# Performance work log

Hardware: AMD Instinct MI355X
Metric: run time of the kernel (lower is better)

The kernel has to match this reference:

```python
import jax, jax.numpy as jnp
import numpy as np

NUM_EXPERTS = 8
TOP_K = 2


def setup_inputs() -> dict:
    key = jax.random.key(0)
    k0, k1, k2, k3, k4 = jax.random.split(key, 5)
    T, D, F, E = 4096, 2048, 4096, NUM_EXPERTS  # tokens, hidden, intermediate, experts
    s_in = 1.0 / np.sqrt(D).astype(np.float32)
    s_mid = 1.0 / np.sqrt(F).astype(np.float32)
    return {
        "hidden_states": jax.random.normal(k0, (T, D), jnp.float32),
        "gate_w": jax.random.normal(k1, (D, E), jnp.float32) * s_in,   # router gate (no bias)
        "w1": jax.random.normal(k2, (E, D, F), jnp.float32) * s_in,     # expert gate proj
        "w3": jax.random.normal(k3, (E, D, F), jnp.float32) * s_in,     # expert up proj
        "w2": jax.random.normal(k4, (E, F, D), jnp.float32) * s_mid,    # expert down proj
    }


def reference(hidden_states, gate_w, w1, w3, w2):
    x = hidden_states  # [T, D] (original flattens any leading dims)
    # Router: logits in fp32 (router_logits.float()), softmax over ALL experts,
    # take top-k WITHOUT renormalization (renormalize=False).
    logits = (x @ gate_w).astype(jnp.float32)            # [T, E]
    probs = jax.nn.softmax(logits, axis=-1)              # [T, E]
    topk_w, topk_i = jax.lax.top_k(probs, TOP_K)         # [T, K]
    # Dense combine weights: zero for non-selected experts. [T, E]
    combine = jnp.sum(
        jax.nn.one_hot(topk_i, NUM_EXPERTS, dtype=x.dtype) * topk_w[..., None],
        axis=1,
    )

    # SwiGLU experts, vmapped over the expert axis (fixed, small E).
    def expert_fn(w1e, w3e, w2e):
        return (jax.nn.silu(x @ w1e) * (x @ w3e)) @ w2e  # [T, D]

    expert_out = jax.vmap(expert_fn)(w1, w3, w2)         # [E, T, D]
    return jnp.einsum("te,etd->td", combine, expert_out)  # [T, D]
```

## Files before the change

### kernel.cpp

```cpp
#include <hip/hip_runtime.h>
#include <hip/hip_bf16.h>

#define TK 4096
#define DD 2048
#define FF 4096
#define NE 8
#define BM 128
#define BN 128
#define BK 32

typedef __attribute__((ext_vector_type(8))) short bf16x8;
typedef __attribute__((ext_vector_type(4))) short bf16x4;
typedef __attribute__((ext_vector_type(4))) float f32x4;

__device__ __forceinline__ unsigned short f2bf(float f) {
  return __builtin_bit_cast(unsigned short, __float2bfloat16(f));
}

__device__ __forceinline__ int g_swz(int row) { return ((row >> 1) & 3) ^ ((row >> 3) & 3); }
__device__ __forceinline__ int swzoff(int row, int bir) {
  return row * 64 + ((((bir >> 4) ^ g_swz(row)) & 3) << 4) + (bir & 15);
}
__device__ __forceinline__ int permB(int f) {
  return (f & 0x60) | ((f & 3) << 3) | ((f >> 2) & 7);
}

__global__ void k_router(const float* __restrict__ x, const float* __restrict__ gw,
                         int* __restrict__ cnt, int* __restrict__ ltok,
                         float* __restrict__ lw) {
  int tok = (blockIdx.x * blockDim.x + threadIdx.x) >> 6;
  int lane = threadIdx.x & 63;
  if (tok >= TK) return;
  const float* xr = x + (size_t)tok * DD;
  float a0=0,a1=0,a2=0,a3=0,a4=0,a5=0,a6=0,a7=0;
  for (int p = 0; p < DD / 256; ++p) {
    int d0 = p * 256 + lane * 4;
    f32x4 xv = *(const f32x4*)(xr + d0);
#pragma unroll
    for (int j = 0; j < 4; ++j) {
      float xs = xv[j];
      const f32x4* g = (const f32x4*)(gw + (size_t)(d0 + j) * NE);
      f32x4 g0 = g[0], g1 = g[1];
      a0 += xs * g0[0]; a1 += xs * g0[1]; a2 += xs * g0[2]; a3 += xs * g0[3];
      a4 += xs * g1[0]; a5 += xs * g1[1]; a6 += xs * g1[2]; a7 += xs * g1[3];
    }
  }
#pragma unroll
  for (int s = 32; s > 0; s >>= 1) {
    a0 += __shfl_xor(a0, s, 64); a1 += __shfl_xor(a1, s, 64);
    a2 += __shfl_xor(a2, s, 64); a3 += __shfl_xor(a3, s, 64);
    a4 += __shfl_xor(a4, s, 64); a5 += __shfl_xor(a5, s, 64);
    a6 += __shfl_xor(a6, s, 64); a7 += __shfl_xor(a7, s, 64);
  }
  if (lane == 0) {
    float p_[NE] = {a0, a1, a2, a3, a4, a5, a6, a7};
    float m = p_[0];
#pragma unroll
    for (int e = 1; e < NE; ++e) m = fmaxf(m, p_[e]);
    float ssum = 0.f;
#pragma unroll
    for (int e = 0; e < NE; ++e) { p_[e] = __expf(p_[e] - m); ssum += p_[e]; }
    float inv = 1.f / ssum;
    int i1 = 0; float b1 = p_[0];
#pragma unroll
    for (int e = 1; e < NE; ++e) if (p_[e] > b1) { b1 = p_[e]; i1 = e; }
    int i2 = -1; float b2 = -1.f;
#pragma unroll
    for (int e = 0; e < NE; ++e) if (e != i1 && p_[e] > b2) { b2 = p_[e]; i2 = e; }
    int s1 = atomicAdd(&cnt[i1], 1);
    ltok[i1 * TK + s1] = tok; lw[i1 * TK + s1] = b1 * inv;
    int s2 = atomicAdd(&cnt[i2], 1);
    ltok[i2 * TK + s2] = tok; lw[i2 * TK + s2] = b2 * inv;
  }
}

__global__ void k_prefix(const int* __restrict__ cnt, int* __restrict__ off) {
  if (threadIdx.x == 0) {
    int a = 0;
#pragma unroll
    for (int e = 0; e < NE; ++e) { off[e] = a; a += cnt[e]; }
    off[NE] = a;
  }
}

__global__ __launch_bounds__(256, 2)
void k_gemm1(const float* __restrict__ x, const float* __restrict__ w1g,
             const float* __restrict__ w3g, const int* __restrict__ cnt,
             const int* __restrict__ off, const int* __restrict__ ltok,
             const float* __restrict__ lw, unsigned short* __restrict__ H) {
  const int e = blockIdx.z;
  const int ce = cnt[e];
  const int m0 = blockIdx.y * BM;
  if (m0 >= ce) return;
  const int n0 = blockIdx.x * BN;
  const int tid = threadIdx.x, lane = tid & 63, wv = tid >> 6;
  const int wr = wv >> 1, wc = wv & 1;
  const float* W1 = w1g + (size_t)e * DD * FF;
  const float* W3 = w3g + (size_t)e * DD * FF;
  const int base = off[e];

  __shared__ unsigned short As[2][BM * BK];
  __shared__ unsigned short B1s[2][BN * BK];
  __shared__ unsigned short B3s[2][BN * BK];

  const int arow = tid >> 1, ah = tid & 1;
  const float* xrow = (m0 + arow < ce) ? (x + (size_t)ltok[e * TK + (m0 + arow)] * DD) : nullptr;
  const int dblk = tid >> 5, fblk = tid & 31;

  const int kb = (lane >> 4) * 16;
  int aOff[4], bOff[4], wAoff[4], wBoff[4];
#pragma unroll
  for (int m = 0; m < 4; ++m) aOff[m] = swzoff(wr * 64 + m * 16 + (lane & 15), kb);
#pragma unroll
  for (int n = 0; n < 4; ++n) bOff[n] = swzoff(permB(wc * 64 + n * 16 + (lane & 15)), kb);
#pragma unroll
  for (int j = 0; j < 4; ++j) {
    wAoff[j] = swzoff(arow, ah * 32 + j * 8);
    wBoff[j] = swzoff(permB(fblk * 4 + j), dblk * 8);
  }

  f32x4 acc1[4][4], acc3[4][4];
#pragma unroll
  for (int m = 0; m < 4; ++m)
#pragma unroll
    for (int n = 0; n < 4; ++n)
#pragma unroll
      for (int j = 0; j < 4; ++j) { acc1[m][n][j] = 0.f; acc3[m][n][j] = 0.f; }

  f32x4 av[4], v1[4], v3[4];

  auto LOAD = [&](int kt) {
    const int k0 = kt * BK;
#pragma unroll
    for (int j = 0; j < 4; ++j) {
      if (xrow) av[j] = *(const f32x4*)(xrow + k0 + ah * 16 + j * 4);
      else { av[j][0] = 0.f; av[j][1] = 0.f; av[j][2] = 0.f; av[j][3] = 0.f; }
    }
    const float* p1 = W1 + (size_t)(k0 + dblk * 4) * FF + (n0 + fblk * 4);
    const float* p3 = W3 + (size_t)(k0 + dblk * 4) * FF + (n0 + fblk * 4);
#pragma unroll
    for (int r = 0; r < 4; ++r) {
      v1[r] = *(const f32x4*)(p1 + (size_t)r * FF);
      v3[r] = *(const f32x4*)(p3 + (size_t)r * FF);
    }
  };
  auto STORE = [&](int buf) {
#pragma unroll
    for (int j = 0; j < 4; ++j) {
      bf16x4 t;
      t[0] = (short)f2bf(av[j][0]); t[1] = (short)f2bf(av[j][1]);
      t[2] = (short)f2bf(av[j][2]); t[3] = (short)f2bf(av[j][3]);
      *(bf16x4*)((char*)As[buf] + wAoff[j]) = t;
    }
#pragma unroll
    for (int j = 0; j < 4; ++j) {
      bf16x4 t1, t3;
      t1[0] = (short)f2bf(v1[0][j]); t1[1] = (short)f2bf(v1[1][j]);
      t1[2] = (short)f2bf(v1[2][j]); t1[3] = (short)f2bf(v1[3][j]);
      t3[0] = (short)f2bf(v3[0][j]); t3[1] = (short)f2bf(v3[1][j]);
      t3[2] = (short)f2bf(v3[2][j]); t3[3] = (short)f2bf(v3[3][j]);
      *(bf16x4*)((char*)B1s[buf] + wBoff[j]) = t1;
      *(bf16x4*)((char*)B3s[buf] + wBoff[j]) = t3;
    }
  };

  LOAD(0);
  STORE(0);
  int cur = 0;
  const int NT = DD / BK;
  for (int kt = 0; kt < NT; ++kt) {
    if (kt + 1 < NT) LOAD(kt + 1);
    __syncthreads();
    bf16x8 af[4];
#pragma unroll
    for (int m = 0; m < 4; ++m) af[m] = *(const bf16x8*)((const char*)As[cur] + aOff[m]);
#pragma unroll
    for (int n = 0; n < 4; ++n) {
      bf16x8 b1 = *(const bf16x8*)((const char*)B1s[cur] + bOff[n]);
      bf16x8 b3 = *(const bf16x8*)((const char*)B3s[cur] + bOff[n]);
#pragma unroll
      for (int m = 0; m < 4; ++m) {
        acc1[m][n] = __builtin_amdgcn_mfma_f32_16x16x32_bf16(af[m], b1, acc1[m][n], 0, 0, 0);
        acc3[m][n] = __builtin_amdgcn_mfma_f32_16x16x32_bf16(af[m], b3, acc3[m][n], 0, 0, 0);
      }
    }
    if (kt + 1 < NT) STORE(cur ^ 1);
    cur ^= 1;
  }

#pragma unroll
  for (int m = 0; m < 4; ++m) {
    const int rbase = wr * 64 + m * 16 + ((lane >> 4) << 2);
    float wts[4]; bool val[4];
#pragma unroll
    for (int j = 0; j < 4; ++j) {
      int r = m0 + rbase + j;
      val[j] = r < ce;
      wts[j] = val[j] ? lw[e * TK + r] : 0.f;
    }
#pragma unroll
    for (int n = 0; n < 4; ++n) {
      const int col = n0 + wc * 64 + n * 16 + (lane & 15);
#pragma unroll
      for (int j = 0; j < 4; ++j) {
        if (!val[j]) continue;
        float s1 = acc1[m][n][j], s3 = acc3[m][n][j];
        float h = s1 / (1.f + __expf(-s1)) * s3 * wts[j];
        H[(size_t)(base + m0 + rbase + j) * FF + col] = f2bf(h);
      }
    }
  }
}

__global__ __launch_bounds__(256, 2)
void k_gemm2(const unsigned short* __restrict__ H, const float* __restrict__ w2g,
             const int* __restrict__ cnt, const int* __restrict__ off,
             const int* __restrict__ ltok, float* __restrict__ out) {
  const int e = blockIdx.z;
  const int ce = cnt[e];
  const int m0 = blockIdx.y * BM;
  if (m0 >= ce) return;
  const int n0 = blockIdx.x * BN;
  const int tid = threadIdx.x, lane = tid & 63, wv = tid >> 6;
  const int wr = wv >> 1, wc = wv & 1;
  const float* W2 = w2g + (size_t)e * FF * DD;
  const int base = off[e];

  __shared__ unsigned short As[2][BM * BK];
  __shared__ unsigned short Bs[2][BN * BK];

  const int arow = tid >> 1, ah = tid & 1;
  const bool aval = (m0 + arow) < ce;
  const unsigned short* hrow = H + (size_t)(base + m0 + arow) * FF;
  const int kblk = tid >> 5, nblk = tid & 31;

  const int kb = (lane >> 4) * 16;
  int aOff[4], bOff[4], wAoff[2], wBoff[4];
#pragma unroll
  for (int m = 0; m < 4; ++m) aOff[m] = swzoff(wr * 64 + m * 16 + (lane & 15), kb);
#pragma unroll
  for (int n = 0; n < 4; ++n) bOff[n] = swzoff(permB(wc * 64 + n * 16 + (lane & 15)), kb);
#pragma unroll
  for (int j = 0; j < 2; ++j) wAoff[j] = swzoff(arow, ah * 32 + j * 16);
#pragma unroll
  for (int j = 0; j < 4; ++j) wBoff[j] = swzoff(permB(nblk * 4 + j), kblk * 8);

  f32x4 acc[4][4];
#pragma unroll
  for (int m = 0; m < 4; ++m)
#pragma unroll
    for (int n = 0; n < 4; ++n)
#pragma unroll
      for (int j = 0; j < 4; ++j) acc[m][n][j] = 0.f;

  bf16x8 av2[2];
  f32x4 wv2[4];

  auto LOAD = [&](int kt) {
    const int k0 = kt * BK;
#pragma unroll
    for (int j = 0; j < 2; ++j) {
      if (aval) av2[j] = *(const bf16x8*)(hrow + k0 + ah * 16 + j * 8);
      else {
#pragma unroll
        for (int q = 0; q < 8; ++q) av2[j][q] = 0;
      }
    }
    const float* p = W2 + (size_t)(k0 + kblk * 4) * DD + (n0 + nblk * 4);
#pragma unroll
    for (int r = 0; r < 4; ++r) wv2[r] = *(const f32x4*)(p + (size_t)r * DD);
  };
  auto STORE = [&](int buf) {
#pragma unroll
    for (int j = 0; j < 2; ++j) *(bf16x8*)((char*)As[buf] + wAoff[j]) = av2[j];
#pragma unroll
    for (int j = 0; j < 4; ++j) {
      bf16x4 t;
      t[0] = (short)f2bf(wv2[0][j]); t[1] = (short)f2bf(wv2[1][j]);
      t[2] = (short)f2bf(wv2[2][j]); t[3] = (short)f2bf(wv2[3][j]);
      *(bf16x4*)((char*)Bs[buf] + wBoff[j]) = t;
    }
  };

  LOAD(0);
  STORE(0);
  int cur = 0;
  const int NT = FF / BK;
  for (int kt = 0; kt < NT; ++kt) {
    if (kt + 1 < NT) LOAD(kt + 1);
    __syncthreads();
    bf16x8 af[4];
#pragma unroll
    for (int m = 0; m < 4; ++m) af[m] = *(const bf16x8*)((const char*)As[cur] + aOff[m]);
#pragma unroll
    for (int n = 0; n < 4; ++n) {
      bf16x8 bf = *(const bf16x8*)((const char*)Bs[cur] + bOff[n]);
#pragma unroll
      for (int m = 0; m < 4; ++m)
        acc[m][n] = __builtin_amdgcn_mfma_f32_16x16x32_bf16(af[m], bf, acc[m][n], 0, 0, 0);
    }
    if (kt + 1 < NT) STORE(cur ^ 1);
    cur ^= 1;
  }

#pragma unroll
  for (int m = 0; m < 4; ++m) {
    const int rbase = wr * 64 + m * 16 + ((lane >> 4) << 2);
    int toks[4]; bool val[4];
#pragma unroll
    for (int j = 0; j < 4; ++j) {
      int r = m0 + rbase + j;
      val[j] = r < ce;
      toks[j] = val[j] ? ltok[e * TK + r] : 0;
    }
#pragma unroll
    for (int n = 0; n < 4; ++n) {
      const int col = n0 + wc * 64 + n * 16 + (lane & 15);
#pragma unroll
      for (int j = 0; j < 4; ++j)
        if (val[j]) atomicAdd(out + (size_t)toks[j] * DD + col, acc[m][n][j]);
    }
  }
}

extern "C" void kernel_launch(void* const* d_in, const int* in_sizes, int n_in,
                              void* d_out, int out_size, void* d_ws, size_t ws_size,
                              hipStream_t stream) {
  const float* x  = (const float*)d_in[0];
  const float* gw = (const float*)d_in[1];
  const float* w1 = (const float*)d_in[2];
  const float* w3 = (const float*)d_in[3];
  const float* w2 = (const float*)d_in[4];
  float* out = (float*)d_out;

  char* ws = (char*)d_ws;
  int*   cnt  = (int*)(ws);
  int*   off  = (int*)(ws + 64);
  int*   ltok = (int*)(ws + 256);
  float* lw   = (float*)(ws + 256 + (size_t)NE * TK * 4);
  unsigned short* H = (unsigned short*)(ws + (1 << 20));
  const size_t need = (1u << 20) + (size_t)2 * TK * FF * 2;
  if (ws_size < need) return;

  hipMemsetAsync(cnt, 0, 64, stream);
  hipMemsetAsync(d_out, 0, (size_t)out_size * 4, stream);
  k_router<<<dim3(TK / 4), 256, 0, stream>>>(x, gw, cnt, ltok, lw);
  k_prefix<<<dim3(1), 64, 0, stream>>>(cnt, off);
  k_gemm1<<<dim3(FF / BN, TK / BM, NE), 256, 0, stream>>>(x, w1, w3, cnt, off, ltok, lw, H);
  k_gemm2<<<dim3(DD / BN, TK / BM, NE), 256, 0, stream>>>(H, w2, cnt, off, ltok, out);
}
```

Before: 981.7 us.

## Pre-convert weights to transposed bf16 and stream tiles via global_load_lds

```diff
diff --git a/kernel.cpp b/kernel.cpp
--- a/kernel.cpp
+++ b/kernel.cpp
@@ -7,7 +7,8 @@
 #define NE 8
 #define BM 128
 #define BN 128
-#define BK 32
+#define BKR 32
+#define BKG 64
 
 typedef __attribute__((ext_vector_type(8))) short bf16x8;
 typedef __attribute__((ext_vector_type(4))) short bf16x4;
@@ -17,6 +18,12 @@
   return __builtin_bit_cast(unsigned short, __float2bfloat16(f));
 }
 
+__device__ __forceinline__ void gl16(const unsigned short* g, unsigned short* l) {
+  __builtin_amdgcn_global_load_lds(
+      (const __attribute__((address_space(1))) unsigned int*)g,
+      (__attribute__((address_space(3))) unsigned int*)l, 16, 0, 0);
+}
+
 __device__ __forceinline__ int g_swz(int row) { return ((row >> 1) & 3) ^ ((row >> 3) & 3); }
 __device__ __forceinline__ int swzoff(int row, int bir) {
   return row * 64 + ((((bir >> 4) ^ g_swz(row)) & 3) << 4) + (bir & 15);
@@ -27,7 +34,7 @@
 
 __global__ void k_router(const float* __restrict__ x, const float* __restrict__ gw,
                          int* __restrict__ cnt, int* __restrict__ ltok,
-                         float* __restrict__ lw) {
+                         float* __restrict__ lw, unsigned short* __restrict__ xb) {
   int tok = (blockIdx.x * blockDim.x + threadIdx.x) >> 6;
   int lane = threadIdx.x & 63;
   if (tok >= TK) return;
@@ -36,6 +43,12 @@
   for (int p = 0; p < DD / 256; ++p) {
     int d0 = p * 256 + lane * 4;
     f32x4 xv = *(const f32x4*)(xr + d0);
+    if (xb) {
+      bf16x4 t;
+      t[0] = (short)f2bf(xv[0]); t[1] = (short)f2bf(xv[1]);
+      t[2] = (short)f2bf(xv[2]); t[3] = (short)f2bf(xv[3]);
+      *(bf16x4*)(xb + (size_t)tok * DD + d0) = t;
+    }
 #pragma unroll
     for (int j = 0; j < 4; ++j) {
       float xs = xv[j];
@@ -80,6 +93,254 @@
 #pragma unroll
     for (int e = 0; e < NE; ++e) { off[e] = a; a += cnt[e]; }
     off[NE] = a;
+  }
+}
+
+__global__ void k_tr(const float* __restrict__ src0, unsigned short* __restrict__ dst0,
+                     int R, int C) {
+  const int e = blockIdx.z;
+  const float* src = src0 + (size_t)e * R * C;
+  unsigned short* dst = dst0 + (size_t)e * R * C;
+  const int r0 = blockIdx.y * 64, c0 = blockIdx.x * 64;
+  const int tid = threadIdx.x;
+  __shared__ unsigned short t[64][66];
+#pragma unroll
+  for (int p = 0; p < 4; ++p) {
+    int r = p * 16 + (tid >> 4);
+    int c = (tid & 15) * 4;
+    f32x4 v = *(const f32x4*)(src + (size_t)(r0 + r) * C + c0 + c);
+#pragma unroll
+    for (int j = 0; j < 4; ++j) t[c + j][r] = f2bf(v[j]);
+  }
+  __syncthreads();
+#pragma unroll
+  for (int p = 0; p < 2; ++p) {
+    int c = p * 32 + (tid >> 3);
+    int r = (tid & 7) * 8;
+    bf16x8 o;
+#pragma unroll
+    for (int j = 0; j < 8; ++j) o[j] = (short)t[c][r + j];
+    *(bf16x8*)(dst + (size_t)(c0 + c) * R + r0 + r) = o;
+  }
+}
+
+
+__global__ __launch_bounds__(256, 2)
+void k_gemm1g(const unsigned short* __restrict__ xb, const unsigned short* __restrict__ w1t,
+              const unsigned short* __restrict__ w3t, const int* __restrict__ cnt,
+              const int* __restrict__ off, const int* __restrict__ ltok,
+              const float* __restrict__ lw, unsigned short* __restrict__ H) {
+  const int e = blockIdx.z;
+  const int ce = cnt[e];
+  const int m0 = blockIdx.y * BM;
+  if (m0 >= ce) return;
+  const int n0 = blockIdx.x * BN;
+  const int tid = threadIdx.x, lane = tid & 63, w = tid >> 6;
+  const int wr = w >> 1, wc = w & 1;
+  const unsigned short* W1 = w1t + (size_t)e * FF * DD;
+  const unsigned short* W3 = w3t + (size_t)e * FF * DD;
+  const int base = off[e];
+
+  __shared__ __align__(16) unsigned short As[BM * BKG];
+  __shared__ __align__(16) unsigned short B1s[BN * BKG];
+  __shared__ __align__(16) unsigned short B3s[BN * BKG];
+
+  const int swz8 = ((lane & 7) ^ ((lane >> 3) & 7)) * 8;
+  const unsigned short* aSrc[4];
+  const unsigned short* b1Src[4];
+  const unsigned short* b3Src[4];
+#pragma unroll
+  for (int i = 0; i < 4; ++i) {
+    int row = w * 32 + i * 8 + (lane >> 3);
+    int gm = m0 + row;
+    int tok = (gm < ce) ? ltok[e * TK + gm] : 0;
+    aSrc[i]  = xb + (size_t)tok * DD + swz8;
+    b1Src[i] = W1 + (size_t)(n0 + row) * DD + swz8;
+    b3Src[i] = W3 + (size_t)(n0 + row) * DD + swz8;
+  }
+
+  int aOff[4][2], bOff[4][2];
+#pragma unroll
+  for (int m = 0; m < 4; ++m) {
+    int row = wr * 64 + m * 16 + (lane & 15);
+#pragma unroll
+    for (int kk = 0; kk < 2; ++kk) {
+      int c = kk * 4 + (lane >> 4);
+      aOff[m][kk] = row * 128 + ((c ^ (row & 7)) << 4);
+    }
+  }
+#pragma unroll
+  for (int n = 0; n < 4; ++n) {
+    int row = wc * 64 + n * 16 + (lane & 15);
+#pragma unroll
+    for (int kk = 0; kk < 2; ++kk) {
+      int c = kk * 4 + (lane >> 4);
+      bOff[n][kk] = row * 128 + ((c ^ (row & 7)) << 4);
+    }
+  }
+
+  f32x4 acc1[4][4], acc3[4][4];
+#pragma unroll
+  for (int m = 0; m < 4; ++m)
+#pragma unroll
+    for (int n = 0; n < 4; ++n)
+#pragma unroll
+      for (int j = 0; j < 4; ++j) { acc1[m][n][j] = 0.f; acc3[m][n][j] = 0.f; }
+
+  const int NT = DD / BKG;
+  for (int kt = 0; kt < NT; ++kt) {
+#pragma unroll
+    for (int i = 0; i < 4; ++i) {
+      const int seg = w * 4 + i;
+      gl16(aSrc[i],  &As[seg * 512]);
+      gl16(b1Src[i], &B1s[seg * 512]);
+      gl16(b3Src[i], &B3s[seg * 512]);
+      aSrc[i] += BKG; b1Src[i] += BKG; b3Src[i] += BKG;
+    }
+    __syncthreads();
+#pragma unroll
+    for (int kk = 0; kk < 2; ++kk) {
+      bf16x8 af[4];
+#pragma unroll
+      for (int m = 0; m < 4; ++m) af[m] = *(const bf16x8*)((const char*)As + aOff[m][kk]);
+#pragma unroll
+      for (int n = 0; n < 4; ++n) {
+        bf16x8 b1 = *(const bf16x8*)((const char*)B1s + bOff[n][kk]);
+        bf16x8 b3 = *(const bf16x8*)((const char*)B3s + bOff[n][kk]);
+#pragma unroll
+        for (int m = 0; m < 4; ++m) {
+          acc1[m][n] = __builtin_amdgcn_mfma_f32_16x16x32_bf16(af[m], b1, acc1[m][n], 0, 0, 0);
+          acc3[m][n] = __builtin_amdgcn_mfma_f32_16x16x32_bf16(af[m], b3, acc3[m][n], 0, 0, 0);
+        }
+      }
+    }
+    __syncthreads();
+  }
+
+#pragma unroll
+  for (int m = 0; m < 4; ++m) {
+    const int rbase = wr * 64 + m * 16 + ((lane >> 4) << 2);
+    float wts[4]; bool val[4];
+#pragma unroll
+    for (int j = 0; j < 4; ++j) {
+      int r = m0 + rbase + j;
+      val[j] = r < ce;
+      wts[j] = val[j] ? lw[e * TK + r] : 0.f;
+    }
+#pragma unroll
+    for (int n = 0; n < 4; ++n) {
+      const int col = n0 + wc * 64 + n * 16 + (lane & 15);
+#pragma unroll
+      for (int j = 0; j < 4; ++j) {
+        if (!val[j]) continue;
+        float s1 = acc1[m][n][j], s3 = acc3[m][n][j];
+        float h = s1 / (1.f + __expf(-s1)) * s3 * wts[j];
+        H[(size_t)(base + m0 + rbase + j) * FF + col] = f2bf(h);
+      }
+    }
+  }
+}
+
+__global__ __launch_bounds__(256, 3)
+void k_gemm2g(const unsigned short* __restrict__ H, const unsigned short* __restrict__ w2t,
+              const int* __restrict__ cnt, const int* __restrict__ off,
+              const int* __restrict__ ltok, float* __restrict__ out) {
+  const int e = blockIdx.z;
+  const int ce = cnt[e];
+  const int m0 = blockIdx.y * BM;
+  if (m0 >= ce) return;
+  const int n0 = blockIdx.x * BN;
+  const int tid = threadIdx.x, lane = tid & 63, w = tid >> 6;
+  const int wr = w >> 1, wc = w & 1;
+  const unsigned short* W2 = w2t + (size_t)e * DD * FF;
+  const int base = off[e];
+
+  __shared__ __align__(16) unsigned short As[BM * BKG];
+  __shared__ __align__(16) unsigned short Bs[BN * BKG];
+
+  const int swz8 = ((lane & 7) ^ ((lane >> 3) & 7)) * 8;
+  const unsigned short* aSrc[4];
+  const unsigned short* bSrc[4];
+#pragma unroll
+  for (int i = 0; i < 4; ++i) {
+    int row = w * 32 + i * 8 + (lane >> 3);
+    int gm = m0 + row;
+    int hr = (gm < ce) ? gm : 0;
+    aSrc[i] = H + (size_t)(base + hr) * FF + swz8;
+    bSrc[i] = W2 + (size_t)(n0 + row) * FF + swz8;
+  }
+
+  int aOff[4][2], bOff[4][2];
+#pragma unroll
+  for (int m = 0; m < 4; ++m) {
+    int row = wr * 64 + m * 16 + (lane & 15);
+#pragma unroll
+    for (int kk = 0; kk < 2; ++kk) {
+      int c = kk * 4 + (lane >> 4);
+      aOff[m][kk] = row * 128 + ((c ^ (row & 7)) << 4);
+    }
+  }
+#pragma unroll
+  for (int n = 0; n < 4; ++n) {
+    int row = wc * 64 + n * 16 + (lane & 15);
+#pragma unroll
+    for (int kk = 0; kk < 2; ++kk) {
+      int c = kk * 4 + (lane >> 4);
+      bOff[n][kk] = row * 128 + ((c ^ (row & 7)) << 4);
+    }
+  }
+
+  f32x4 acc[4][4];
+#pragma unroll
+  for (int m = 0; m < 4; ++m)
+#pragma unroll
+    for (int n = 0; n < 4; ++n)
+#pragma unroll
+      for (int j = 0; j < 4; ++j) acc[m][n][j] = 0.f;
+
+  const int NT = FF / BKG;
+  for (int kt = 0; kt < NT; ++kt) {
+#pragma unroll
+    for (int i = 0; i < 4; ++i) {
+      const int seg = w * 4 + i;
+      gl16(aSrc[i], &As[seg * 512]);
+      gl16(bSrc[i], &Bs[seg * 512]);
+      aSrc[i] += BKG; bSrc[i] += BKG;
+    }
+    __syncthreads();
+#pragma unroll
+    for (int kk = 0; kk < 2; ++kk) {
+      bf16x8 af[4];
+#pragma unroll
+      for (int m = 0; m < 4; ++m) af[m] = *(const bf16x8*)((const char*)As + aOff[m][kk]);
+#pragma unroll
+      for (int n = 0; n < 4; ++n) {
+        bf16x8 bf = *(const bf16x8*)((const char*)Bs + bOff[n][kk]);
+#pragma unroll
+        for (int m = 0; m < 4; ++m)
+          acc[m][n] = __builtin_amdgcn_mfma_f32_16x16x32_bf16(af[m], bf, acc[m][n], 0, 0, 0);
+      }
+    }
+    __syncthreads();
+  }
+
+#pragma unroll
+  for (int m = 0; m < 4; ++m) {
+    const int rbase = wr * 64 + m * 16 + ((lane >> 4) << 2);
+    int toks[4]; bool val[4];
+#pragma unroll
+    for (int j = 0; j < 4; ++j) {
+      int r = m0 + rbase + j;
+      val[j] = r < ce;
+      toks[j] = val[j] ? ltok[e * TK + r] : 0;
+    }
+#pragma unroll
+    for (int n = 0; n < 4; ++n) {
+      const int col = n0 + wc * 64 + n * 16 + (lane & 15);
+#pragma unroll
+      for (int j = 0; j < 4; ++j)
+        if (val[j]) atomicAdd(out + (size_t)toks[j] * DD + col, acc[m][n][j]);
+    }
   }
 }
 
@@ -99,9 +360,9 @@
   const float* W3 = w3g + (size_t)e * DD * FF;
   const int base = off[e];
 
-  __shared__ unsigned short As[2][BM * BK];
-  __shared__ unsigned short B1s[2][BN * BK];
-  __shared__ unsigned short B3s[2][BN * BK];
+  __shared__ unsigned short As[2][BM * BKR];
+  __shared__ unsigned short B1s[2][BN * BKR];
+  __shared__ unsigned short B3s[2][BN * BKR];
 
   const int arow = tid >> 1, ah = tid & 1;
   const float* xrow = (m0 + arow < ce) ? (x + (size_t)ltok[e * TK + (m0 + arow)] * DD) : nullptr;
@@ -130,7 +391,7 @@
   f32x4 av[4], v1[4], v3[4];
 
   auto LOAD = [&](int kt) {
-    const int k0 = kt * BK;
+    const int k0 = kt * BKR;
 #pragma unroll
     for (int j = 0; j < 4; ++j) {
       if (xrow) av[j] = *(const f32x4*)(xrow + k0 + ah * 16 + j * 4);
@@ -164,10 +425,9 @@
     }
   };
 
-  LOAD(0);
-  STORE(0);
+  LOAD(0); STORE(0);
   int cur = 0;
-  const int NT = DD / BK;
+  const int NT = DD / BKR;
   for (int kt = 0; kt < NT; ++kt) {
     if (kt + 1 < NT) LOAD(kt + 1);
     __syncthreads();
@@ -226,8 +486,8 @@
   const float* W2 = w2g + (size_t)e * FF * DD;
   const int base = off[e];
 
-  __shared__ unsigned short As[2][BM * BK];
-  __shared__ unsigned short Bs[2][BN * BK];
+  __shared__ unsigned short As[2][BM * BKR];
+  __shared__ unsigned short Bs[2][BN * BKR];
 
   const int arow = tid >> 1, ah = tid & 1;
   const bool aval = (m0 + arow) < ce;
@@ -257,7 +517,7 @@
   f32x4 wv2[4];
 
   auto LOAD = [&](int kt) {
-    const int k0 = kt * BK;
+    const int k0 = kt * BKR;
 #pragma unroll
     for (int j = 0; j < 2; ++j) {
       if (aval) av2[j] = *(const bf16x8*)(hrow + k0 + ah * 16 + j * 8);
@@ -282,10 +542,9 @@
     }
   };
 
-  LOAD(0);
-  STORE(0);
+  LOAD(0); STORE(0);
   int cur = 0;
-  const int NT = FF / BK;
+  const int NT = FF / BKR;
   for (int kt = 0; kt < NT; ++kt) {
     if (kt + 1 < NT) LOAD(kt + 1);
     __syncthreads();
@@ -338,14 +597,35 @@
   int*   off  = (int*)(ws + 64);
   int*   ltok = (int*)(ws + 256);
   float* lw   = (float*)(ws + 256 + (size_t)NE * TK * 4);
-  unsigned short* H = (unsigned short*)(ws + (1 << 20));
-  const size_t need = (1u << 20) + (size_t)2 * TK * FF * 2;
-  if (ws_size < need) return;
+
+  const size_t SZ_XB = (size_t)TK * DD * 2;
+  const size_t SZ_W  = (size_t)NE * DD * FF * 2;
+  const size_t SZ_H  = (size_t)2 * TK * FF * 2;
+  size_t o = (size_t)1 << 20;
+  unsigned short* xb  = (unsigned short*)(ws + o); o += SZ_XB;
+  unsigned short* w1t = (unsigned short*)(ws + o); o += SZ_W;
+  unsigned short* w3t = (unsigned short*)(ws + o); o += SZ_W;
+  unsigned short* w2t = (unsigned short*)(ws + o); o += SZ_W;
+  unsigned short* Hg  = (unsigned short*)(ws + o); o += SZ_H;
+  const bool full = (ws_size >= o);
 
   hipMemsetAsync(cnt, 0, 64, stream);
   hipMemsetAsync(d_out, 0, (size_t)out_size * 4, stream);
-  k_router<<<dim3(TK / 4), 256, 0, stream>>>(x, gw, cnt, ltok, lw);
-  k_prefix<<<dim3(1), 64, 0, stream>>>(cnt, off);
-  k_gemm1<<<dim3(FF / BN, TK / BM, NE), 256, 0, stream>>>(x, w1, w3, cnt, off, ltok, lw, H);
-  k_gemm2<<<dim3(DD / BN, TK / BM, NE), 256, 0, stream>>>(H, w2, cnt, off, ltok, out);
-}
+
+  if (full) {
+    k_router<<<dim3(TK / 4), 256, 0, stream>>>(x, gw, cnt, ltok, lw, xb);
+    k_prefix<<<dim3(1), 64, 0, stream>>>(cnt, off);
+    k_tr<<<dim3(FF / 64, DD / 64, NE), 256, 0, stream>>>(w1, w1t, DD, FF);
+    k_tr<<<dim3(FF / 64, DD / 64, NE), 256, 0, stream>>>(w3, w3t, DD, FF);
+    k_tr<<<dim3(DD / 64, FF / 64, NE), 256, 0, stream>>>(w2, w2t, FF, DD);
+    k_gemm1g<<<dim3(FF / BN, TK / BM, NE), 256, 0, stream>>>(xb, w1t, w3t, cnt, off, ltok, lw, Hg);
+    k_gemm2g<<<dim3(DD / BN, TK / BM, NE), 256, 0, stream>>>(Hg, w2t, cnt, off, ltok, out);
+  } else {
+    unsigned short* H = (unsigned short*)(ws + ((size_t)1 << 20));
+    if (ws_size < ((size_t)1 << 20) + SZ_H) return;
+    k_router<<<dim3(TK / 4), 256, 0, stream>>>(x, gw, cnt, ltok, lw, (unsigned short*)nullptr);
+    k_prefix<<<dim3(1), 64, 0, stream>>>(cnt, off);
+    k_gemm1<<<dim3(FF / BN, TK / BM, NE), 256, 0, stream>>>(x, w1, w3, cnt, off, ltok, lw, H);
+    k_gemm2<<<dim3(DD / BN, TK / BM, NE), 256, 0, stream>>>(H, w2, cnt, off, ltok, out);
+  }
+}
```

Result: no change. 962.9 us (-1.9%).
